# Kernel optimization log

Measured on AMD Instinct MI355X. Metric: run time of the kernel, lower is better.

Reference implementation:

```python
import jax, jax.numpy as jnp
import numpy as np

N = 100000   # nodes
E = 1000000  # edges
F_IN = 64    # num_node_features
H = 64       # hidden_channels
G = 64       # graphs in batch
OUT = 1


def setup_inputs() -> dict:
    key = jax.random.key(0)
    ks = jax.random.split(key, 16)
    inp = {}
    inp['x'] = jax.random.normal(ks[0], (N, F_IN), dtype=jnp.float32)
    inp['edge_index'] = jax.random.randint(ks[1], (2, E), 0, N, dtype=jnp.int64)
    inp['batch'] = jnp.sort(jax.random.randint(ks[2], (N,), 0, G, dtype=jnp.int64))
    s_in = 1.0 / np.sqrt(F_IN)
    s_h = 1.0 / np.sqrt(H)
    # GraphConv 1: in=F_IN -> H  (lin_rel has bias, lin_root has no bias)
    inp['W1r'] = jax.random.uniform(ks[3], (F_IN, H), jnp.float32, -s_in, s_in)
    inp['b1'] = jax.random.uniform(ks[4], (H,), jnp.float32, -s_in, s_in)
    inp['W1o'] = jax.random.uniform(ks[5], (F_IN, H), jnp.float32, -s_in, s_in)
    # GraphConv 2, 3: H -> H
    inp['W2r'] = jax.random.uniform(ks[6], (H, H), jnp.float32, -s_h, s_h)
    inp['b2'] = jax.random.uniform(ks[7], (H,), jnp.float32, -s_h, s_h)
    inp['W2o'] = jax.random.uniform(ks[8], (H, H), jnp.float32, -s_h, s_h)
    inp['W3r'] = jax.random.uniform(ks[9], (H, H), jnp.float32, -s_h, s_h)
    inp['b3'] = jax.random.uniform(ks[10], (H,), jnp.float32, -s_h, s_h)
    inp['W3o'] = jax.random.uniform(ks[11], (H, H), jnp.float32, -s_h, s_h)
    # PReLU slopes (num_parameters=1, init=0.25)
    inp['a1'] = jnp.array(0.25, dtype=jnp.float32)
    inp['a2'] = jnp.array(0.25, dtype=jnp.float32)
    # head
    inp['W_lin0'] = jax.random.uniform(ks[12], (H, H), jnp.float32, -s_h, s_h)
    inp['b_lin0'] = jax.random.uniform(ks[13], (H,), jnp.float32, -s_h, s_h)
    inp['W_lin1'] = jax.random.uniform(ks[14], (H, OUT), jnp.float32, -s_h, s_h)
    inp['b_lin1'] = jax.random.uniform(ks[15], (OUT,), jnp.float32, -s_h, s_h)
    return inp


def _graph_conv(x, src, dst, Wr, b, Wo):
    # PyG GraphConv, aggr='add': out_i = Wr @ (sum_{j->i} x_j) + Wo @ x_i + b.
    # Aggregate raw features first (linear commutes with sum) -> one small GEMM.
    agg = jax.ops.segment_sum(x[src], dst, num_segments=N)  # [N, d_in]
    return agg @ Wr + x @ Wo + b


def _prelu(x, a):
    return jnp.where(x >= 0, x, a * x)


def reference(x, edge_index, batch, W1r, b1, W1o, W2r, b2, W2o, W3r, b3, W3o,
              a1, a2, W_lin0, b_lin0, W_lin1, b_lin1):
    src, dst = edge_index[0], edge_index[1]
    h = _graph_conv(x, src, dst, W1r, b1, W1o)
    h = _prelu(h, a1)  # dropout is identity in eval mode
    h = _graph_conv(h, src, dst, W2r, b2, W2o)
    h = _prelu(h, a2)
    h = _graph_conv(h, src, dst, W3r, b3, W3o)
    # global_mean_pool over graph ids
    sums = jax.ops.segment_sum(h, batch, num_segments=G)            # [G, H]
    cnts = jax.ops.segment_sum(jnp.ones((N,), h.dtype), batch, num_segments=G)
    pooled = sums / jnp.maximum(cnts, 1.0)[:, None]
    out = pooled @ W_lin0 + b_lin0
    out = out @ W_lin1 + b_lin1
    return out  # [G, OUT]
```

## Files before the change

### kernel.cpp

```cpp
#include <hip/hip_runtime.h>

#define FDIM 64
#define POOL_CHUNK 32
#define ECAP 512
#define NBK_SHIFT 8
#define BCAP 4096
#define CHUNK 8192

typedef unsigned int uint32;
typedef unsigned short ushort16;
typedef __attribute__((ext_vector_type(8))) short bf8v;
typedef __attribute__((ext_vector_type(4))) float f4v;

static inline size_t align_up(size_t v) { return (v + 255) & ~(size_t)255; }

__device__ __forceinline__ float bcastf(float v, int l) {
    return __int_as_float(__builtin_amdgcn_readlane(__float_as_int(v), l));
}
__device__ __forceinline__ float bf_lo(uint32 u) { return __uint_as_float(u << 16); }
__device__ __forceinline__ float bf_hi(uint32 u) { return __uint_as_float(u & 0xFFFF0000u); }
__device__ __forceinline__ unsigned short f2bf(float f) {
    uint32 u = __float_as_uint(f);
    return (unsigned short)((u + 0x7FFFu + ((u >> 16) & 1u)) >> 16);
}
__device__ __forceinline__ float bf2f(unsigned short s) {
    return __uint_as_float(((uint32)s) << 16);
}


__global__ __launch_bounds__(256) void k_bhist(const int* __restrict__ dst,
                                               int* __restrict__ bcount, int E, int nb) {
    __shared__ int h[512];
    for (int i = threadIdx.x; i < nb; i += 256) h[i] = 0;
    __syncthreads();
    int stride = gridDim.x * blockDim.x;
    for (int e = blockIdx.x * blockDim.x + threadIdx.x; e < E; e += stride)
        atomicAdd(&h[dst[e] >> NBK_SHIFT], 1);
    __syncthreads();
    for (int i = threadIdx.x; i < nb; i += 256)
        if (h[i]) atomicAdd(&bcount[i], h[i]);
}

__global__ __launch_bounds__(512) void k_bscan(const int* __restrict__ bcount,
                                               int* __restrict__ bbase,
                                               int* __restrict__ bcursor, int nb,
                                               int* __restrict__ rowstart, int n, int E) {
    __shared__ int sh[512];
    int t = threadIdx.x;
    int v = (t < nb) ? bcount[t] : 0;
    sh[t] = v;
    __syncthreads();
    for (int off = 1; off < 512; off <<= 1) {
        int a = (t >= off) ? sh[t - off] : 0;
        __syncthreads();
        sh[t] += a;
        __syncthreads();
    }
    if (t < nb) { int ex = sh[t] - v; bbase[t] = ex; bcursor[t] = ex; }
    if (t == 0) { bbase[nb] = E; rowstart[n] = E; }
}

__global__ __launch_bounds__(1024) void k_bgroup(const int* __restrict__ src,
                                                 const int* __restrict__ dst,
                                                 int* __restrict__ bcursor,
                                                 uint32* __restrict__ ebuf, int E, int nb) {
    __shared__ uint32 sorted[CHUNK];
    __shared__ unsigned short bop[CHUNK];
    __shared__ int hist[512];
    __shared__ int gbase[512];
    __shared__ int cur[512];
    __shared__ int sh[512];
    int c0 = blockIdx.x * CHUNK;
    int cend = c0 + CHUNK; if (cend > E) cend = E;
    int cnt = cend - c0;
    int t = threadIdx.x;
    for (int i = t; i < nb; i += 1024) hist[i] = 0;
    __syncthreads();
    for (int i = t; i < cnt; i += 1024)
        atomicAdd(&hist[dst[c0 + i] >> NBK_SHIFT], 1);
    __syncthreads();
    int v = 0;
    if (t < 512) { v = (t < nb) ? hist[t] : 0; sh[t] = v; }
    __syncthreads();
    for (int off = 1; off < 512; off <<= 1) {
        int a = (t >= off && t < 512) ? sh[t - off] : 0;
        __syncthreads();
        if (t < 512) sh[t] += a;
        __syncthreads();
    }
    if (t < nb) {
        int lofs = sh[t] - v;
        cur[t] = lofs;
        hist[t] = lofs;
        gbase[t] = v ? atomicAdd(&bcursor[t], v) : 0;
    }
    __syncthreads();
    for (int i = t; i < cnt; i += 1024) {
        int d = dst[c0 + i], s = src[c0 + i];
        int b = d >> NBK_SHIFT;
        int p = atomicAdd(&cur[b], 1);
        sorted[p] = ((uint32)(d & ((1 << NBK_SHIFT) - 1)) << 24) | (uint32)s;
        bop[p] = (unsigned short)b;
    }
    __syncthreads();
    for (int i = t; i < cnt; i += 1024) {
        int b = bop[i];
        ebuf[gbase[b] + (i - hist[b])] = sorted[i];
    }
}

__global__ __launch_bounds__(256) void k_blocal(const uint32* __restrict__ ebuf,
                                                const int* __restrict__ bbase,
                                                int* __restrict__ rowstart,
                                                int* __restrict__ adj, int n) {
    __shared__ uint32 raw[BCAP];
    __shared__ int srt[BCAP];
    __shared__ int hist[257];
    __shared__ int cur[256];
    int b = blockIdx.x;
    int t = threadIdx.x;
    int lo = bbase[b], hi = bbase[b + 1];
    int cnt = hi - lo;
    for (int i = t; i < 257; i += 256) hist[i] = 0;
    __syncthreads();
    if (cnt <= BCAP) {
        for (int i = t; i < cnt; i += 256) {
            uint32 v = ebuf[lo + i];
            raw[i] = v;
            atomicAdd(&hist[(v >> 24) + 1], 1);
        }
        __syncthreads();
        {
            for (int off = 1; off < 256; off <<= 1) {
                int a = (t >= off) ? hist[t + 1 - off] : 0;
                __syncthreads();
                hist[t + 1] += a;
                __syncthreads();
            }
        }
        if (t < 256) cur[t] = hist[t];
        __syncthreads();
        for (int i = t; i < cnt; i += 256) {
            uint32 v = raw[i];
            int p = atomicAdd(&cur[v >> 24], 1);
            srt[p] = (int)(v & 0xFFFFFF);
        }
        __syncthreads();
        for (int i = t; i < cnt; i += 256) adj[lo + i] = srt[i];
    } else {
        for (int i = t; i < cnt; i += 256) {
            uint32 v = ebuf[lo + i];
            atomicAdd(&hist[(v >> 24) + 1], 1);
        }
        __syncthreads();
        {
            for (int off = 1; off < 256; off <<= 1) {
                int a = (t >= off) ? hist[t + 1 - off] : 0;
                __syncthreads();
                hist[t + 1] += a;
                __syncthreads();
            }
        }
        if (t < 256) cur[t] = hist[t];
        __syncthreads();
        for (int i = t; i < cnt; i += 256) {
            uint32 v = ebuf[lo + i];
            int p = atomicAdd(&cur[v >> 24], 1);
            adj[lo + p] = (int)(v & 0xFFFFFF);
        }
    }
    if (t < 256) {
        int node = (b << NBK_SHIFT) + t;
        if (node < n) rowstart[node] = lo + hist[t];
    }
}


__global__ void k_cvt(const float* __restrict__ in, ushort16* __restrict__ out, long n4) {
    long i = (long)blockIdx.x * blockDim.x + threadIdx.x;
    long stride = (long)gridDim.x * blockDim.x;
    for (; i < n4; i += stride) {
        float4 v = ((const float4*)in)[i];
        uint2 o;
        o.x = (uint32)f2bf(v.x) | ((uint32)f2bf(v.y) << 16);
        o.y = (uint32)f2bf(v.z) | ((uint32)f2bf(v.w) << 16);
        ((uint2*)out)[i] = o;
    }
}


__global__ __launch_bounds__(1024) void k_layer(
    const ushort16* __restrict__ Hbf, const int* __restrict__ rowstart,
    const int* __restrict__ adj, const float* __restrict__ Wr,
    const float* __restrict__ Wo, const float* __restrict__ bias,
    const float* __restrict__ slope_p, ushort16* __restrict__ HbfOut,
    int n, int do_prelu)
{
    __shared__ unsigned short wh[64 * 128];
    __shared__ unsigned short wl[64 * 128];
    __shared__ int eidx[16][ECAP];

    for (int e = threadIdx.x; e < 64 * 128; e += 1024) {
        int nn = e >> 7;
        int k  = e & 127;
        float v = (k < 64) ? Wr[k * 64 + nn] : Wo[(k - 64) * 64 + nn];
        unsigned short hi = f2bf(v);
        unsigned short lo = f2bf(v - bf2f(hi));
        int boff = nn * 256 + ((k * 2) ^ ((nn & 7) << 4));
        wh[boff >> 1] = hi;
        wl[boff >> 1] = lo;
    }
    __syncthreads();

    int lane  = threadIdx.x & 63;
    int l15   = lane & 15;
    int kg    = lane >> 4;
    int koff  = kg * 8;
    int wslot = threadIdx.x >> 6;
    int wid  = (blockIdx.x * blockDim.x + threadIdx.x) >> 6;
    int nw   = (gridDim.x * blockDim.x) >> 6;
    int ntiles = (n + 15) >> 4;
    float slope = do_prelu ? slope_p[0] : 1.0f;
    float bv0 = bias[l15], bv1 = bias[16 + l15], bv2 = bias[32 + l15], bv3 = bias[48 + l15];

    for (int t = wid; t < ntiles; t += nw) {
        int base16 = t * 16;
        int node = base16 + l15;
        bool valid = node < n;
        int s0 = valid ? rowstart[node] : 0;
        int s1 = valid ? rowstart[node + 1] : 0;
        int ebase = __builtin_amdgcn_readlane(s0, 0);
        int eend  = __builtin_amdgcn_readlane(s1, 15);
        if (!valid) { s0 = 0; s1 = 0; }
        if (base16 + 16 > n) eend = rowstart[n];
        int ecount = eend - ebase;

        int cap = ecount < ECAP ? ecount : ECAP;
        for (int i = lane; i < cap; i += 64) eidx[wslot][i] = adj[ebase + i];
        asm volatile("s_waitcnt lgkmcnt(0)" ::: "memory");

        int4 su = {0, 0, 0, 0}, sv = {0, 0, 0, 0};
        if (valid) {
            const ushort16* sp = Hbf + ((long)node << 6);
            su = *(const int4*)(sp + koff);
            sv = *(const int4*)(sp + koff + 32);
        }

        float acc[16];
#pragma unroll
        for (int i = 0; i < 16; i++) acc[i] = 0.f;

#define ACC8(UU, BASE) \
        acc[BASE+0] += bf_lo(UU.x); acc[BASE+1] += bf_hi(UU.x); \
        acc[BASE+2] += bf_lo(UU.y); acc[BASE+3] += bf_hi(UU.y); \
        acc[BASE+4] += bf_lo(UU.z); acc[BASE+5] += bf_hi(UU.z); \
        acc[BASE+6] += bf_lo(UU.w); acc[BASE+7] += bf_hi(UU.w);

        if (ecount <= ECAP) {
            int ls0 = s0 - ebase, ls1 = s1 - ebase;
            const int* ix = eidx[wslot];
            int j = ls0;
            for (; j + 4 <= ls1; j += 4) {
                long r0 = ix[j], r1 = ix[j + 1], r2 = ix[j + 2], r3 = ix[j + 3];
                const ushort16* p0 = Hbf + (r0 << 6);
                const ushort16* p1 = Hbf + (r1 << 6);
                const ushort16* p2 = Hbf + (r2 << 6);
                const ushort16* p3 = Hbf + (r3 << 6);
                int4 u0 = *(const int4*)(p0 + koff), v0 = *(const int4*)(p0 + koff + 32);
                int4 u1 = *(const int4*)(p1 + koff), v1 = *(const int4*)(p1 + koff + 32);
                int4 u2 = *(const int4*)(p2 + koff), v2 = *(const int4*)(p2 + koff + 32);
                int4 u3 = *(const int4*)(p3 + koff), v3 = *(const int4*)(p3 + koff + 32);
                ACC8(u0, 0)  ACC8(u1, 0)  ACC8(u2, 0)  ACC8(u3, 0)
                ACC8(v0, 8)  ACC8(v1, 8)  ACC8(v2, 8)  ACC8(v3, 8)
            }
            for (; j < ls1; j++) {
                long r0 = ix[j];
                const ushort16* p0 = Hbf + (r0 << 6);
                int4 u0 = *(const int4*)(p0 + koff), v0 = *(const int4*)(p0 + koff + 32);
                ACC8(u0, 0)  ACC8(v0, 8)
            }
        } else {
            for (int e = s0; e < s1; e++) {
                long r0 = adj[e];
                const ushort16* p0 = Hbf + (r0 << 6);
                int4 u0 = *(const int4*)(p0 + koff), v0 = *(const int4*)(p0 + koff + 32);
                ACC8(u0, 0)  ACC8(v0, 8)
            }
        }
#undef ACC8

        bf8v ah[4], al[2];
#pragma unroll
        for (int kb = 0; kb < 2; kb++) {
#pragma unroll
            for (int j = 0; j < 8; j++) {
                float v = acc[kb * 8 + j];
                unsigned short h = f2bf(v);
                ah[kb][j] = (short)h;
                al[kb][j] = (short)f2bf(v - bf2f(h));
            }
        }
        ah[2] = __builtin_bit_cast(bf8v, su);
        ah[3] = __builtin_bit_cast(bf8v, sv);

        f4v C[4];
        C[0] = (f4v){bv0, bv0, bv0, bv0};
        C[1] = (f4v){bv1, bv1, bv1, bv1};
        C[2] = (f4v){bv2, bv2, bv2, bv2};
        C[3] = (f4v){bv3, bv3, bv3, bv3};

#pragma unroll
        for (int kb = 0; kb < 4; kb++) {
#pragma unroll
            for (int nt = 0; nt < 4; nt++) {
                int row = nt * 16 + l15;
                int boff = row * 256 + (((kb * 32 + kg * 8) * 2) ^ ((l15 & 7) << 4));
                bf8v bh = *(const bf8v*)((const char*)wh + boff);
                bf8v bl = *(const bf8v*)((const char*)wl + boff);
                C[nt] = __builtin_amdgcn_mfma_f32_16x16x32_bf16(ah[kb], bh, C[nt], 0, 0, 0);
                if (kb < 2)
                    C[nt] = __builtin_amdgcn_mfma_f32_16x16x32_bf16(al[kb], bh, C[nt], 0, 0, 0);
                C[nt] = __builtin_amdgcn_mfma_f32_16x16x32_bf16(ah[kb], bl, C[nt], 0, 0, 0);
            }
        }

#pragma unroll
        for (int r = 0; r < 4; r++) {
            int onode = base16 + kg * 4 + r;
            if (onode < n) {
#pragma unroll
                for (int nt = 0; nt < 4; nt++) {
                    float v = C[nt][r];
                    v = v >= 0.f ? v : slope * v;
                    HbfOut[((long)onode << 6) + nt * 16 + l15] = f2bf(v);
                }
            }
        }
    }
}


__global__ __launch_bounds__(256) void k_pool(const ushort16* __restrict__ h,
                                              const int* __restrict__ batch,
                                              float* __restrict__ sums,
                                              float* __restrict__ cnt, int n) {
    int wave = (blockIdx.x * 256 + threadIdx.x) >> 6;
    int lane = threadIdx.x & 63;
    int start = wave * POOL_CHUNK;
    if (start >= n) return;
    int end = start + POOL_CHUNK;
    if (end > n) end = n;
    int cur = batch[start];
    float acc = 0.f;
    int count = 0;
#pragma unroll 4
    for (int i = start; i < end; i++) {
        int g = batch[i];
        if (g != cur) {
            atomicAdd(&sums[cur * FDIM + lane], acc);
            if (lane == 0) atomicAdd(&cnt[cur], (float)count);
            acc = 0.f;
            count = 0;
            cur = g;
        }
        acc += bf2f(h[(long)i * FDIM + lane]);
        count++;
    }
    atomicAdd(&sums[cur * FDIM + lane], acc);
    if (lane == 0) atomicAdd(&cnt[cur], (float)count);
}


__global__ __launch_bounds__(64) void k_head(const float* __restrict__ sums,
                                             const float* __restrict__ cnt,
                                             const float* __restrict__ W0,
                                             const float* __restrict__ b0,
                                             const float* __restrict__ W1,
                                             const float* __restrict__ b1,
                                             float* __restrict__ out, int OUT) {
    int g = blockIdx.x;
    int lane = threadIdx.x;
    float c = cnt[g];
    if (c < 1.f) c = 1.f;
    float p = sums[g * FDIM + lane] / c;

    float h0 = 0.f, h1 = 0.f, h2 = 0.f, h3 = 0.f;
#pragma unroll
    for (int k = 0; k < FDIM; k += 4) {
        h0 += bcastf(p, k + 0) * W0[(k + 0) * FDIM + lane];
        h1 += bcastf(p, k + 1) * W0[(k + 1) * FDIM + lane];
        h2 += bcastf(p, k + 2) * W0[(k + 2) * FDIM + lane];
        h3 += bcastf(p, k + 3) * W0[(k + 3) * FDIM + lane];
    }
    float hid = b0[lane] + ((h0 + h1) + (h2 + h3));
    for (int o = 0; o < OUT; o++) {
        float part = hid * W1[lane * OUT + o];
#pragma unroll
        for (int m = 32; m >= 1; m >>= 1) part += __shfl_xor(part, m, 64);
        if (lane == 0) out[g * OUT + o] = part + b1[o];
    }
}

extern "C" void kernel_launch(void* const* d_in, const int* in_sizes, int n_in,
                              void* d_out, int out_size, void* d_ws, size_t ws_size,
                              hipStream_t stream) {
    const float* x     = (const float*)d_in[0];
    const int*   ei    = (const int*)d_in[1];
    const int*   batch = (const int*)d_in[2];
    const float* W1r = (const float*)d_in[3];
    const float* b1  = (const float*)d_in[4];
    const float* W1o = (const float*)d_in[5];
    const float* W2r = (const float*)d_in[6];
    const float* b2  = (const float*)d_in[7];
    const float* W2o = (const float*)d_in[8];
    const float* W3r = (const float*)d_in[9];
    const float* b3  = (const float*)d_in[10];
    const float* W3o = (const float*)d_in[11];
    const float* a1  = (const float*)d_in[12];
    const float* a2  = (const float*)d_in[13];
    const float* Wl0 = (const float*)d_in[14];
    const float* bl0 = (const float*)d_in[15];
    const float* Wl1 = (const float*)d_in[16];
    const float* bl1 = (const float*)d_in[17];

    int N = in_sizes[0] / FDIM;
    int E = in_sizes[1] / 2;
    int OUT = in_sizes[17];
    int G = out_size / OUT;
    int nb = (N + 255) >> NBK_SHIFT;

    const int* src = ei;
    const int* dst = ei + E;

    char* w = (char*)d_ws;
    int* rowstart = (int*)w;              w += align_up((size_t)(N + 1) * 4);
    int* adj      = (int*)w;              w += align_up((size_t)E * 4 + 256);
    uint32* ebuf  = (uint32*)w;           w += align_up((size_t)E * 4);
    int* bbase    = (int*)w;              w += align_up((size_t)(nb + 1) * 4);
    int* bcursor  = (int*)w;              w += align_up((size_t)nb * 4);
    ushort16* xbf = (ushort16*)w;         w += align_up((size_t)N * FDIM * 2);
    ushort16* hb1 = (ushort16*)w;         w += align_up((size_t)N * FDIM * 2);
    ushort16* hb2 = (ushort16*)w;         w += align_up((size_t)N * FDIM * 2);
    ushort16* hb3 = (ushort16*)w;         w += align_up((size_t)N * FDIM * 2);
    char* zbase   = w;
    int* bcount   = (int*)w;              w += align_up(512 * 4);
    float* sums   = (float*)w;            w += align_up((size_t)G * FDIM * 4);
    float* cnt    = (float*)w;            w += align_up((size_t)G * 4);

    hipMemsetAsync(zbase, 0, (size_t)(w - zbase), stream);

    k_bhist<<<512, 256, 0, stream>>>(dst, bcount, E, nb);
    k_bscan<<<1, 512, 0, stream>>>(bcount, bbase, bcursor, nb, rowstart, N, E);
    int nchunks = (E + CHUNK - 1) / CHUNK;
    k_bgroup<<<nchunks, 1024, 0, stream>>>(src, dst, bcursor, ebuf, E, nb);
    k_blocal<<<nb, 256, 0, stream>>>(ebuf, bbase, rowstart, adj, N);

    k_cvt<<<1024, 256, 0, stream>>>(x, xbf, (long)N * FDIM / 4);

    int ntiles = (N + 15) / 16;
    int layerGrid = (ntiles + 15) / 16;
    k_layer<<<layerGrid, 1024, 0, stream>>>(xbf, rowstart, adj, W1r, W1o, b1, a1, hb1, N, 1);
    k_layer<<<layerGrid, 1024, 0, stream>>>(hb1, rowstart, adj, W2r, W2o, b2, a2, hb2, N, 1);
    k_layer<<<layerGrid, 1024, 0, stream>>>(hb2, rowstart, adj, W3r, W3o, b3, nullptr, hb3, N, 0);

    int poolWaves = (N + POOL_CHUNK - 1) / POOL_CHUNK;
    int poolGrid = (poolWaves + 3) / 4;
    k_pool<<<poolGrid, 256, 0, stream>>>(hb3, batch, sums, cnt, N);
    k_head<<<G, 64, 0, stream>>>(sums, cnt, Wl0, bl0, Wl1, bl1, (float*)d_out, OUT);
}
```

Measured before the change: 205.8 us.

## Fuse pooling into last layer, fold bf16 conversion into histogram, retune CSR build

The global mean pool now runs inside the third GraphConv kernel: each wave accumulates its output rows per graph id and atomically adds them into the sums buffer. This removes the hb3 buffer, its write and re-read, and the separate pool launch. The x-to-bf16 conversion moves into the edge histogram kernel, node counts come from a binary search over the sorted batch array in the head kernel, and the CSR build gets a smaller CHUNK and 512-thread local sort blocks. The cost is more global float atomics from the last layer, and per-graph counts now rely on batch being sorted.

```diff
diff --git a/kernel.cpp b/kernel.cpp
--- a/kernel.cpp
+++ b/kernel.cpp
@@ -1,11 +1,10 @@
 #include <hip/hip_runtime.h>
 
 #define FDIM 64
-#define POOL_CHUNK 32
 #define ECAP 512
 #define NBK_SHIFT 8
 #define BCAP 4096
-#define CHUNK 8192
+#define CHUNK 4096
 
 typedef unsigned int uint32;
 typedef unsigned short ushort16;
@@ -29,12 +28,22 @@
 
 
 __global__ __launch_bounds__(256) void k_bhist(const int* __restrict__ dst,
-                                               int* __restrict__ bcount, int E, int nb) {
+                                               int* __restrict__ bcount, int E, int nb,
+                                               const float* __restrict__ xin,
+                                               ushort16* __restrict__ xbf, long n4) {
     __shared__ int h[512];
     for (int i = threadIdx.x; i < nb; i += 256) h[i] = 0;
     __syncthreads();
-    int stride = gridDim.x * blockDim.x;
-    for (int e = blockIdx.x * blockDim.x + threadIdx.x; e < E; e += stride)
+    long stride = (long)gridDim.x * blockDim.x;
+    long tid = (long)blockIdx.x * blockDim.x + threadIdx.x;
+    for (long i = tid; i < n4; i += stride) {
+        float4 v = ((const float4*)xin)[i];
+        uint2 o;
+        o.x = (uint32)f2bf(v.x) | ((uint32)f2bf(v.y) << 16);
+        o.y = (uint32)f2bf(v.z) | ((uint32)f2bf(v.w) << 16);
+        ((uint2*)xbf)[i] = o;
+    }
+    for (long e = tid; e < E; e += stride)
         atomicAdd(&h[dst[e] >> NBK_SHIFT], 1);
     __syncthreads();
     for (int i = threadIdx.x; i < nb; i += 256)
@@ -109,7 +118,7 @@
     }
 }
 
-__global__ __launch_bounds__(256) void k_blocal(const uint32* __restrict__ ebuf,
+__global__ __launch_bounds__(512) void k_blocal(const uint32* __restrict__ ebuf,
                                                 const int* __restrict__ bbase,
                                                 int* __restrict__ rowstart,
                                                 int* __restrict__ adj, int n) {
@@ -121,49 +130,45 @@
     int t = threadIdx.x;
     int lo = bbase[b], hi = bbase[b + 1];
     int cnt = hi - lo;
-    for (int i = t; i < 257; i += 256) hist[i] = 0;
+    for (int i = t; i < 257; i += 512) hist[i] = 0;
     __syncthreads();
     if (cnt <= BCAP) {
-        for (int i = t; i < cnt; i += 256) {
+        for (int i = t; i < cnt; i += 512) {
             uint32 v = ebuf[lo + i];
             raw[i] = v;
             atomicAdd(&hist[(v >> 24) + 1], 1);
         }
         __syncthreads();
-        {
-            for (int off = 1; off < 256; off <<= 1) {
-                int a = (t >= off) ? hist[t + 1 - off] : 0;
-                __syncthreads();
-                hist[t + 1] += a;
-                __syncthreads();
-            }
+        for (int off = 1; off < 256; off <<= 1) {
+            int a = (t >= off && t < 256) ? hist[t + 1 - off] : 0;
+            __syncthreads();
+            if (t < 256) hist[t + 1] += a;
+            __syncthreads();
         }
         if (t < 256) cur[t] = hist[t];
         __syncthreads();
-        for (int i = t; i < cnt; i += 256) {
+        for (int i = t; i < cnt; i += 512) {
             uint32 v = raw[i];
             int p = atomicAdd(&cur[v >> 24], 1);
             srt[p] = (int)(v & 0xFFFFFF);
         }
         __syncthreads();
-        for (int i = t; i < cnt; i += 256) adj[lo + i] = srt[i];
+        for (int i = t; i < cnt; i += 512) adj[lo + i] = srt[i];
     } else {
-        for (int i = t; i < cnt; i += 256) {
+        for (int i = t; i < cnt; i += 512) {
             uint32 v = ebuf[lo + i];
             atomicAdd(&hist[(v >> 24) + 1], 1);
         }
         __syncthreads();
-        {
-            for (int off = 1; off < 256; off <<= 1) {
-                int a = (t >= off) ? hist[t + 1 - off] : 0;
-                __syncthreads();
-                hist[t + 1] += a;
-                __syncthreads();
-            }
+        for (int off = 1; off < 256; off <<= 1) {
+            int a = (t >= off && t < 256) ? hist[t + 1 - off] : 0;
+            __syncthreads();
+            if (t < 256) hist[t + 1] += a;
+            __syncthreads();
         }
         if (t < 256) cur[t] = hist[t];
         __syncthreads();
-        for (int i = t; i < cnt; i += 256) {
+        for (int i = t; i < cnt; i += 512) {
             uint32 v = ebuf[lo + i];
             int p = atomicAdd(&cur[v >> 24], 1);
             adj[lo + p] = (int)(v & 0xFFFFFF);
@@ -176,25 +181,13 @@
 }
 
 
-__global__ void k_cvt(const float* __restrict__ in, ushort16* __restrict__ out, long n4) {
-    long i = (long)blockIdx.x * blockDim.x + threadIdx.x;
-    long stride = (long)gridDim.x * blockDim.x;
-    for (; i < n4; i += stride) {
-        float4 v = ((const float4*)in)[i];
-        uint2 o;
-        o.x = (uint32)f2bf(v.x) | ((uint32)f2bf(v.y) << 16);
-        o.y = (uint32)f2bf(v.z) | ((uint32)f2bf(v.w) << 16);
-        ((uint2*)out)[i] = o;
-    }
-}
-
-
-__global__ __launch_bounds__(1024) void k_layer(
+template<int DO_POOL>
+__global__ __launch_bounds__(1024, 8) void k_layer(
     const ushort16* __restrict__ Hbf, const int* __restrict__ rowstart,
     const int* __restrict__ adj, const float* __restrict__ Wr,
     const float* __restrict__ Wo, const float* __restrict__ bias,
     const float* __restrict__ slope_p, ushort16* __restrict__ HbfOut,
-    int n, int do_prelu)
+    int n, int do_prelu, const int* __restrict__ batch, float* __restrict__ sums)
 {
     __shared__ unsigned short wh[64 * 128];
     __shared__ unsigned short wl[64 * 128];
@@ -324,55 +317,52 @@
             }
         }
 
-#pragma unroll
-        for (int r = 0; r < 4; r++) {
-            int onode = base16 + kg * 4 + r;
-            if (onode < n) {
-#pragma unroll
-                for (int nt = 0; nt < 4; nt++) {
-                    float v = C[nt][r];
-                    v = v >= 0.f ? v : slope * v;
-                    HbfOut[((long)onode << 6) + nt * 16 + l15] = f2bf(v);
+        if (!DO_POOL) {
+#pragma unroll
+            for (int r = 0; r < 4; r++) {
+                int onode = base16 + kg * 4 + r;
+                if (onode < n) {
+#pragma unroll
+                    for (int nt = 0; nt < 4; nt++) {
+                        float v = C[nt][r];
+                        v = v >= 0.f ? v : slope * v;
+                        HbfOut[((long)onode << 6) + nt * 16 + l15] = f2bf(v);
+                    }
                 }
             }
-        }
-    }
-}
-
-
-__global__ __launch_bounds__(256) void k_pool(const ushort16* __restrict__ h,
-                                              const int* __restrict__ batch,
-                                              float* __restrict__ sums,
-                                              float* __restrict__ cnt, int n) {
-    int wave = (blockIdx.x * 256 + threadIdx.x) >> 6;
-    int lane = threadIdx.x & 63;
-    int start = wave * POOL_CHUNK;
-    if (start >= n) return;
-    int end = start + POOL_CHUNK;
-    if (end > n) end = n;
-    int cur = batch[start];
-    float acc = 0.f;
-    int count = 0;
-#pragma unroll 4
-    for (int i = start; i < end; i++) {
-        int g = batch[i];
-        if (g != cur) {
-            atomicAdd(&sums[cur * FDIM + lane], acc);
-            if (lane == 0) atomicAdd(&cnt[cur], (float)count);
-            acc = 0.f;
-            count = 0;
-            cur = g;
-        }
-        acc += bf2f(h[(long)i * FDIM + lane]);
-        count++;
-    }
-    atomicAdd(&sums[cur * FDIM + lane], acc);
-    if (lane == 0) atomicAdd(&cnt[cur], (float)count);
+        } else {
+            int curg = -1;
+            float a0 = 0.f, a1 = 0.f, a2 = 0.f, a3 = 0.f;
+#pragma unroll
+            for (int r = 0; r < 4; r++) {
+                int onode = base16 + kg * 4 + r;
+                if (onode < n) {
+                    int g = batch[onode];
+                    if (g != curg) {
+                        if (curg >= 0) {
+                            atomicAdd(&sums[curg * FDIM +  0 + l15], a0);
+                            atomicAdd(&sums[curg * FDIM + 16 + l15], a1);
+                            atomicAdd(&sums[curg * FDIM + 32 + l15], a2);
+                            atomicAdd(&sums[curg * FDIM + 48 + l15], a3);
+                        }
+                        curg = g; a0 = a1 = a2 = a3 = 0.f;
+                    }
+                    a0 += C[0][r]; a1 += C[1][r]; a2 += C[2][r]; a3 += C[3][r];
+                }
+            }
+            if (curg >= 0) {
+                atomicAdd(&sums[curg * FDIM +  0 + l15], a0);
+                atomicAdd(&sums[curg * FDIM + 16 + l15], a1);
+                atomicAdd(&sums[curg * FDIM + 32 + l15], a2);
+                atomicAdd(&sums[curg * FDIM + 48 + l15], a3);
+            }
+        }
+    }
 }
 
 
 __global__ __launch_bounds__(64) void k_head(const float* __restrict__ sums,
-                                             const float* __restrict__ cnt,
+                                             const int* __restrict__ batch, int n,
                                              const float* __restrict__ W0,
                                              const float* __restrict__ b0,
                                              const float* __restrict__ W1,
@@ -380,7 +370,11 @@
                                              float* __restrict__ out, int OUT) {
     int g = blockIdx.x;
     int lane = threadIdx.x;
-    float c = cnt[g];
+    int lo = 0, hi = n;
+    while (lo < hi) { int m = (lo + hi) >> 1; if (batch[m] < g) lo = m + 1; else hi = m; }
+    int lo2 = lo, hi2 = n;
+    while (lo2 < hi2) { int m = (lo2 + hi2) >> 1; if (batch[m] <= g) lo2 = m + 1; else hi2 = m; }
+    float c = (float)(lo2 - lo);
     if (c < 1.f) c = 1.f;
     float p = sums[g * FDIM + lane] / c;
 
@@ -441,30 +435,23 @@
     ushort16* xbf = (ushort16*)w;         w += align_up((size_t)N * FDIM * 2);
     ushort16* hb1 = (ushort16*)w;         w += align_up((size_t)N * FDIM * 2);
     ushort16* hb2 = (ushort16*)w;         w += align_up((size_t)N * FDIM * 2);
-    ushort16* hb3 = (ushort16*)w;         w += align_up((size_t)N * FDIM * 2);
     char* zbase   = w;
     int* bcount   = (int*)w;              w += align_up(512 * 4);
     float* sums   = (float*)w;            w += align_up((size_t)G * FDIM * 4);
-    float* cnt    = (float*)w;            w += align_up((size_t)G * 4);
 
     hipMemsetAsync(zbase, 0, (size_t)(w - zbase), stream);
 
-    k_bhist<<<512, 256, 0, stream>>>(dst, bcount, E, nb);
+    k_bhist<<<512, 256, 0, stream>>>(dst, bcount, E, nb, x, xbf, (long)N * FDIM / 4);
     k_bscan<<<1, 512, 0, stream>>>(bcount, bbase, bcursor, nb, rowstart, N, E);
     int nchunks = (E + CHUNK - 1) / CHUNK;
     k_bgroup<<<nchunks, 1024, 0, stream>>>(src, dst, bcursor, ebuf, E, nb);
-    k_blocal<<<nb, 256, 0, stream>>>(ebuf, bbase, rowstart, adj, N);
-
-    k_cvt<<<1024, 256, 0, stream>>>(x, xbf, (long)N * FDIM / 4);
+    k_blocal<<<nb, 512, 0, stream>>>(ebuf, bbase, rowstart, adj, N);
 
     int ntiles = (N + 15) / 16;
     int layerGrid = (ntiles + 15) / 16;
-    k_layer<<<layerGrid, 1024, 0, stream>>>(xbf, rowstart, adj, W1r, W1o, b1, a1, hb1, N, 1);
-    k_layer<<<layerGrid, 1024, 0, stream>>>(hb1, rowstart, adj, W2r, W2o, b2, a2, hb2, N, 1);
-    k_layer<<<layerGrid, 1024, 0, stream>>>(hb2, rowstart, adj, W3r, W3o, b3, nullptr, hb3, N, 0);
-
-    int poolWaves = (N + POOL_CHUNK - 1) / POOL_CHUNK;
-    int poolGrid = (poolWaves + 3) / 4;
-    k_pool<<<poolGrid, 256, 0, stream>>>(hb3, batch, sums, cnt, N);
-    k_head<<<G, 64, 0, stream>>>(sums, cnt, Wl0, bl0, Wl1, bl1, (float*)d_out, OUT);
-}
+    k_layer<0><<<layerGrid, 1024, 0, stream>>>(xbf, rowstart, adj, W1r, W1o, b1, a1, hb1, N, 1, nullptr, nullptr);
+    k_layer<0><<<layerGrid, 1024, 0, stream>>>(hb1, rowstart, adj, W2r, W2o, b2, a2, hb2, N, 1, nullptr, nullptr);
+    k_layer<1><<<layerGrid, 1024, 0, stream>>>(hb2, rowstart, adj, W3r, W3o, b3, nullptr, hb1, N, 0, batch, sums);
+
+    k_head<<<G, 64, 0, stream>>>(sums, batch, N, Wl0, bl0, Wl1, bl1, (float*)d_out, OUT);
+}
```

After: 437.6 us. 2.13x slower.
